# Performance work log

Hardware: AMD Instinct MI355X
Metric: run time of the kernel (lower is better)

## Reference

```python
import jax, jax.numpy as jnp
import numpy as np

B, S, D = 16, 2048, 128

def setup_inputs() -> dict:
    key = jax.random.key(0)
    kq, kk, kv = jax.random.split(key, 3)
    Q = jax.random.normal(kq, (B, S, D), dtype=jnp.float32)
    K = jax.random.normal(kk, (B, S, D), dtype=jnp.float32)
    V = jax.random.normal(kv, (B, S, D), dtype=jnp.float32)
    mask = jnp.ones((B, S), dtype=jnp.int32)  # key padding mask; 0 = masked out
    return {"Q": Q, "K": K, "V": V, "mask": mask}

def reference(Q, K, V, mask):
    scale = jnp.asarray(D ** 0.5, dtype=Q.dtype)
    # scores: [B, Sq, Sk]
    scores = jnp.einsum('bqd,bkd->bqk', Q, K) / scale
    neg_inf = jnp.asarray(float('-inf'), dtype=scores.dtype)
    # mask==0 -> -inf, broadcast over query dim: [B, 1, Sk]
    scores = jnp.where((mask == 0)[:, None, :], neg_inf, scores)
    attn = jax.nn.softmax(scores, axis=-1)
    out = jnp.einsum('bqk,bkd->bqd', attn, V)
    return (out, attn)
```

## Files before the change

kernel.cpp:

```cpp
#include <hip/hip_runtime.h>

#define BB 16
#define SS 2048
#define DD 128
#define SCALE 0.08838834764831845f

typedef __attribute__((ext_vector_type(8))) short bf16x8;
typedef __attribute__((ext_vector_type(4))) float f32x4;

__device__ __forceinline__ unsigned short f2bf(float f) {
    union { float f; unsigned int u; } v; v.f = f;
    unsigned int u = v.u;
    return (unsigned short)((u + 0x7fffu + ((u >> 16) & 1u)) >> 16);
}

__global__ __launch_bounds__(256) void cvt_bf16_kernel(const float* __restrict__ src,
                                                       unsigned short* __restrict__ dst) {
    int idx = (blockIdx.x * 256 + threadIdx.x) * 4;
    float4 f = *(const float4*)(src + idx);
    ushort4 o;
    o.x = f2bf(f.x); o.y = f2bf(f.y); o.z = f2bf(f.z); o.w = f2bf(f.w);
    *(ushort4*)(dst + idx) = o;
}

__global__ __launch_bounds__(256) void transpose_v_kernel(const float* __restrict__ v,
                                                          unsigned short* __restrict__ vt) {
    __shared__ unsigned short sT[64 * 132];
    int b = blockIdx.x >> 5;
    int s0 = (blockIdx.x & 31) * 64;
    int tid = threadIdx.x;
#pragma unroll
    for (int rnd = 0; rnd < 8; ++rnd) {
        int slot = rnd * 256 + tid;
        int row = slot >> 5;
        int c4 = (slot & 31) * 4;
        float4 f = *(const float4*)(v + (size_t)(b * SS + s0 + row) * DD + c4);
        unsigned short* p = &sT[row * 132 + c4];
        p[0] = f2bf(f.x); p[1] = f2bf(f.y); p[2] = f2bf(f.z); p[3] = f2bf(f.w);
    }
    __syncthreads();
#pragma unroll
    for (int rnd = 0; rnd < 4; ++rnd) {
        int slot = rnd * 256 + tid;
        int d = slot >> 3;
        int k8 = (slot & 7) * 8;
        __align__(16) unsigned short tmp[8];
#pragma unroll
        for (int e = 0; e < 8; ++e) tmp[e] = sT[(k8 + e) * 132 + d];
        *(ushort4*)(vt + (size_t)(b * DD + d) * SS + s0 + k8) = *(ushort4*)&tmp[0];
        *(ushort4*)(vt + (size_t)(b * DD + d) * SS + s0 + k8 + 4) = *(ushort4*)&tmp[4];
    }
}

__global__ __launch_bounds__(256) void attn_kernel(const unsigned short* __restrict__ Qb,
                                                   const unsigned short* __restrict__ Kb,
                                                   const unsigned short* __restrict__ Vt,
                                                   const int* __restrict__ mask,
                                                   float* __restrict__ outO,
                                                   float* __restrict__ outA) {
    __shared__ unsigned short sQ[64 * 136];
    __shared__ unsigned short sK[64 * 136];
    __shared__ unsigned short sV[128 * 72];
    __shared__ unsigned short sP[64 * 72];
    __shared__ float sLpart[2][64];
    __shared__ float sLinv[64];
    __shared__ float sMsk[64];

    int bi = blockIdx.x;
    int slot = bi >> 3;
    int b = (bi & 7) * 2 + (slot >> 5);
    int qt = slot & 31;

    int tid = threadIdx.x;
    int wave = tid >> 6, lane = tid & 63, lo = lane & 15, hi = lane >> 4;

    const unsigned short* Qbase = Qb + (size_t)(b * SS + qt * 64) * DD;
#pragma unroll
    for (int rnd = 0; rnd < 4; ++rnd) {
        int sl = rnd * 256 + tid;
        int row = sl >> 4, coff = (sl & 15) * 8;
        *(int4*)&sQ[row * 136 + coff] = *(const int4*)(Qbase + row * DD + coff);
    }
    if (tid < 64) { sLpart[0][tid] = 0.f; sLpart[1][tid] = 0.f; }

    const int r0 = (wave >> 1) * 32;
    const int c0 = (wave & 1) * 32;

    for (int kt = 0; kt < 32; ++kt) {
        __syncthreads();
        const unsigned short* Kbase = Kb + (size_t)(b * SS + kt * 64) * DD;
#pragma unroll
        for (int rnd = 0; rnd < 4; ++rnd) {
            int sl = rnd * 256 + tid;
            int row = sl >> 4, coff = (sl & 15) * 8;
            *(int4*)&sK[row * 136 + coff] = *(const int4*)(Kbase + row * DD + coff);
        }
        if (tid < 64) sMsk[tid] = mask[b * SS + kt * 64 + tid] ? 1.f : 0.f;
        __syncthreads();

        f32x4 acc[2][2];
#pragma unroll
        for (int ii = 0; ii < 2; ++ii)
#pragma unroll
            for (int jj = 0; jj < 2; ++jj) acc[ii][jj] = (f32x4){0.f, 0.f, 0.f, 0.f};
#pragma unroll
        for (int ks = 0; ks < 4; ++ks) {
            bf16x8 af[2], bf[2];
#pragma unroll
            for (int ii = 0; ii < 2; ++ii)
                af[ii] = *(const bf16x8*)&sQ[(r0 + ii * 16 + lo) * 136 + ks * 32 + hi * 8];
#pragma unroll
            for (int jj = 0; jj < 2; ++jj)
                bf[jj] = *(const bf16x8*)&sK[(c0 + jj * 16 + lo) * 136 + ks * 32 + hi * 8];
#pragma unroll
            for (int ii = 0; ii < 2; ++ii)
#pragma unroll
                for (int jj = 0; jj < 2; ++jj)
                    acc[ii][jj] = __builtin_amdgcn_mfma_f32_16x16x32_bf16(af[ii], bf[jj], acc[ii][jj], 0, 0, 0);
        }
        float m0 = sMsk[c0 + lo], m1 = sMsk[c0 + 16 + lo];
#pragma unroll
        for (int ii = 0; ii < 2; ++ii) {
#pragma unroll
            for (int r = 0; r < 4; ++r) {
                float v = __expf(acc[ii][0][r] * SCALE) * m0 + __expf(acc[ii][1][r] * SCALE) * m1;
                v += __shfl_xor(v, 1);
                v += __shfl_xor(v, 2);
                v += __shfl_xor(v, 4);
                v += __shfl_xor(v, 8);
                if (lo == 0) sLpart[wave & 1][r0 + ii * 16 + hi * 4 + r] += v;
            }
        }
    }
    __syncthreads();
    if (tid < 64) sLinv[tid] = 1.f / (sLpart[0][tid] + sLpart[1][tid]);

    f32x4 oacc[4][2];
#pragma unroll
    for (int mi = 0; mi < 4; ++mi)
#pragma unroll
        for (int tj = 0; tj < 2; ++tj) oacc[mi][tj] = (f32x4){0.f, 0.f, 0.f, 0.f};
    const int dv0 = wave * 32;

    for (int kt = 0; kt < 32; ++kt) {
        __syncthreads();
        const unsigned short* Kbase = Kb + (size_t)(b * SS + kt * 64) * DD;
#pragma unroll
        for (int rnd = 0; rnd < 4; ++rnd) {
            int sl = rnd * 256 + tid;
            int row = sl >> 4, coff = (sl & 15) * 8;
            *(int4*)&sK[row * 136 + coff] = *(const int4*)(Kbase + row * DD + coff);
        }
#pragma unroll
        for (int rnd = 0; rnd < 4; ++rnd) {
            int sl = rnd * 256 + tid;
            int row = sl >> 3, koff = (sl & 7) * 8;
            *(int4*)&sV[row * 72 + koff] =
                *(const int4*)(Vt + (size_t)(b * DD + row) * SS + kt * 64 + koff);
        }
        if (tid < 64) sMsk[tid] = mask[b * SS + kt * 64 + tid] ? 1.f : 0.f;
        __syncthreads();

        f32x4 acc[2][2];
#pragma unroll
        for (int ii = 0; ii < 2; ++ii)
#pragma unroll
            for (int jj = 0; jj < 2; ++jj) acc[ii][jj] = (f32x4){0.f, 0.f, 0.f, 0.f};
#pragma unroll
        for (int ks = 0; ks < 4; ++ks) {
            bf16x8 af[2], bf[2];
#pragma unroll
            for (int ii = 0; ii < 2; ++ii)
                af[ii] = *(const bf16x8*)&sQ[(r0 + ii * 16 + lo) * 136 + ks * 32 + hi * 8];
#pragma unroll
            for (int jj = 0; jj < 2; ++jj)
                bf[jj] = *(const bf16x8*)&sK[(c0 + jj * 16 + lo) * 136 + ks * 32 + hi * 8];
#pragma unroll
            for (int ii = 0; ii < 2; ++ii)
#pragma unroll
                for (int jj = 0; jj < 2; ++jj)
                    acc[ii][jj] = __builtin_amdgcn_mfma_f32_16x16x32_bf16(af[ii], bf[jj], acc[ii][jj], 0, 0, 0);
        }
        float m01[2] = {sMsk[c0 + lo], sMsk[c0 + 16 + lo]};
#pragma unroll
        for (int ii = 0; ii < 2; ++ii) {
#pragma unroll
            for (int jj = 0; jj < 2; ++jj) {
#pragma unroll
                for (int r = 0; r < 4; ++r) {
                    int row = r0 + ii * 16 + hi * 4 + r;
                    int col = c0 + jj * 16 + lo;
                    float p = __expf(acc[ii][jj][r] * SCALE) * m01[jj] * sLinv[row];
                    outA[(size_t)(b * SS + qt * 64 + row) * SS + kt * 64 + col] = p;
                    sP[row * 72 + col] = f2bf(p);
                }
            }
        }
        __syncthreads();

#pragma unroll
        for (int ks = 0; ks < 2; ++ks) {
            bf16x8 pa[4], vb[2];
#pragma unroll
            for (int mi = 0; mi < 4; ++mi)
                pa[mi] = *(const bf16x8*)&sP[(mi * 16 + lo) * 72 + ks * 32 + hi * 8];
#pragma unroll
            for (int tj = 0; tj < 2; ++tj)
                vb[tj] = *(const bf16x8*)&sV[(dv0 + tj * 16 + lo) * 72 + ks * 32 + hi * 8];
#pragma unroll
            for (int mi = 0; mi < 4; ++mi)
#pragma unroll
                for (int tj = 0; tj < 2; ++tj)
                    oacc[mi][tj] = __builtin_amdgcn_mfma_f32_16x16x32_bf16(pa[mi], vb[tj], oacc[mi][tj], 0, 0, 0);
        }
    }

#pragma unroll
    for (int mi = 0; mi < 4; ++mi) {
#pragma unroll
        for (int tj = 0; tj < 2; ++tj) {
#pragma unroll
            for (int r = 0; r < 4; ++r) {
                int row = mi * 16 + hi * 4 + r;
                int dv = dv0 + tj * 16 + lo;
                outO[(size_t)(b * SS + qt * 64 + row) * DD + dv] = oacc[mi][tj][r];
            }
        }
    }
}

extern "C" void kernel_launch(void* const* d_in, const int* in_sizes, int n_in,
                              void* d_out, int out_size, void* d_ws, size_t ws_size,
                              hipStream_t stream) {
    const float* Q = (const float*)d_in[0];
    const float* K = (const float*)d_in[1];
    const float* V = (const float*)d_in[2];
    const int* mask = (const int*)d_in[3];

    float* outO = (float*)d_out;
    float* outA = outO + (size_t)BB * SS * DD;

    unsigned short* Qb = (unsigned short*)d_ws;
    unsigned short* Kb = Qb + (size_t)BB * SS * DD;
    unsigned short* Vt = Kb + (size_t)BB * SS * DD;

    int nconv = (BB * SS * DD) / (256 * 4);
    cvt_bf16_kernel<<<nconv, 256, 0, stream>>>(Q, Qb);
    cvt_bf16_kernel<<<nconv, 256, 0, stream>>>(K, Kb);
    transpose_v_kernel<<<BB * (SS / 64), 256, 0, stream>>>(V, Vt);
    attn_kernel<<<BB * (SS / 64), 256, 0, stream>>>(Qb, Kb, Vt, mask, outO, outA);
}
```

Before: 458.5 us.

## Fuse prep kernels, halve query tile, prefetch K/V tiles in registers

Merges the three preprocessing launches into a single prep kernel. The attention kernel's query tile shrinks from 64 to 32 rows, doubling the grid to 1024 blocks, and shared memory is aliased to allow three blocks per CU. The next K and V tiles are loaded into registers while the current tile is computed. Row-sum reductions now stay in registers until the end of the pass, and mask values are read directly from global memory. The main aim is more occupancy and latency hiding on a kernel dominated by writing the attention matrix, at the cost of reading K and V twice as often in total.

```diff
diff --git a/kernel.cpp b/kernel.cpp
--- a/kernel.cpp
+++ b/kernel.cpp
@@ -14,27 +14,34 @@
     return (unsigned short)((u + 0x7fffu + ((u >> 16) & 1u)) >> 16);
 }
 
-__global__ __launch_bounds__(256) void cvt_bf16_kernel(const float* __restrict__ src,
-                                                       unsigned short* __restrict__ dst) {
-    int idx = (blockIdx.x * 256 + threadIdx.x) * 4;
-    float4 f = *(const float4*)(src + idx);
-    ushort4 o;
-    o.x = f2bf(f.x); o.y = f2bf(f.y); o.z = f2bf(f.z); o.w = f2bf(f.w);
-    *(ushort4*)(dst + idx) = o;
-}
-
-__global__ __launch_bounds__(256) void transpose_v_kernel(const float* __restrict__ v,
-                                                          unsigned short* __restrict__ vt) {
+__global__ __launch_bounds__(256) void prep_kernel(const float* __restrict__ Q,
+                                                   const float* __restrict__ K,
+                                                   const float* __restrict__ V,
+                                                   unsigned short* __restrict__ Qb,
+                                                   unsigned short* __restrict__ Kb,
+                                                   unsigned short* __restrict__ Vt) {
+    int bid = blockIdx.x;
+    int tid = threadIdx.x;
+    if (bid < 8192) {
+        const float* src = (bid < 4096) ? Q : K;
+        unsigned short* dst = (bid < 4096) ? Qb : Kb;
+        int idx = ((bid & 4095) * 256 + tid) * 4;
+        float4 f = *(const float4*)(src + idx);
+        ushort4 o;
+        o.x = f2bf(f.x); o.y = f2bf(f.y); o.z = f2bf(f.z); o.w = f2bf(f.w);
+        *(ushort4*)(dst + idx) = o;
+        return;
+    }
     __shared__ unsigned short sT[64 * 132];
-    int b = blockIdx.x >> 5;
-    int s0 = (blockIdx.x & 31) * 64;
-    int tid = threadIdx.x;
+    int tb = bid - 8192;
+    int b = tb >> 5;
+    int s0 = (tb & 31) * 64;
 #pragma unroll
     for (int rnd = 0; rnd < 8; ++rnd) {
         int slot = rnd * 256 + tid;
         int row = slot >> 5;
         int c4 = (slot & 31) * 4;
-        float4 f = *(const float4*)(v + (size_t)(b * SS + s0 + row) * DD + c4);
+        float4 f = *(const float4*)(V + (size_t)(b * SS + s0 + row) * DD + c4);
         unsigned short* p = &sT[row * 132 + c4];
         p[0] = f2bf(f.x); p[1] = f2bf(f.y); p[2] = f2bf(f.z); p[3] = f2bf(f.w);
     }
@@ -47,183 +54,213 @@
         __align__(16) unsigned short tmp[8];
 #pragma unroll
         for (int e = 0; e < 8; ++e) tmp[e] = sT[(k8 + e) * 132 + d];
-        *(ushort4*)(vt + (size_t)(b * DD + d) * SS + s0 + k8) = *(ushort4*)&tmp[0];
-        *(ushort4*)(vt + (size_t)(b * DD + d) * SS + s0 + k8 + 4) = *(ushort4*)&tmp[4];
-    }
-}
-
-__global__ __launch_bounds__(256) void attn_kernel(const unsigned short* __restrict__ Qb,
-                                                   const unsigned short* __restrict__ Kb,
-                                                   const unsigned short* __restrict__ Vt,
-                                                   const int* __restrict__ mask,
-                                                   float* __restrict__ outO,
-                                                   float* __restrict__ outA) {
-    __shared__ unsigned short sQ[64 * 136];
-    __shared__ unsigned short sK[64 * 136];
-    __shared__ unsigned short sV[128 * 72];
-    __shared__ unsigned short sP[64 * 72];
-    __shared__ float sLpart[2][64];
-    __shared__ float sLinv[64];
-    __shared__ float sMsk[64];
+        *(ushort4*)(Vt + (size_t)(b * DD + d) * SS + s0 + k8) = *(ushort4*)&tmp[0];
+        *(ushort4*)(Vt + (size_t)(b * DD + d) * SS + s0 + k8 + 4) = *(ushort4*)&tmp[4];
+    }
+}
+
+__global__ __launch_bounds__(256, 3) void attn_kernel(const unsigned short* __restrict__ Qb,
+                                                      const unsigned short* __restrict__ Kb,
+                                                      const unsigned short* __restrict__ Vt,
+                                                      const int* __restrict__ mask,
+                                                      float* __restrict__ outO,
+                                                      float* __restrict__ outA) {
+    __shared__ __align__(16) char smem[44544];
+    unsigned short* sQ = (unsigned short*)smem;
+    unsigned short* sK = (unsigned short*)(smem + 8704);
+    unsigned short* sP = sK;
+    unsigned short* sV = (unsigned short*)(smem + 8704 + 17408);
+    float* sLpart = (float*)sV;
 
     int bi = blockIdx.x;
     int slot = bi >> 3;
-    int b = (bi & 7) * 2 + (slot >> 5);
-    int qt = slot & 31;
+    int b = (bi & 7) * 2 + (slot >> 6);
+    int qt = slot & 63;
 
     int tid = threadIdx.x;
     int wave = tid >> 6, lane = tid & 63, lo = lane & 15, hi = lane >> 4;
-
-    const unsigned short* Qbase = Qb + (size_t)(b * SS + qt * 64) * DD;
-#pragma unroll
-    for (int rnd = 0; rnd < 4; ++rnd) {
+    const int r0 = (wave >> 1) * 16;
+    const int c0 = (wave & 1) * 32;
+
+    const unsigned short* KbB = Kb + (size_t)b * SS * DD;
+    const unsigned short* VtB = Vt + (size_t)b * DD * SS;
+    const int* maskB = mask + b * SS;
+
+    const unsigned short* Qbase = Qb + (size_t)(b * SS + qt * 32) * DD;
+#pragma unroll
+    for (int rnd = 0; rnd < 2; ++rnd) {
         int sl = rnd * 256 + tid;
         int row = sl >> 4, coff = (sl & 15) * 8;
         *(int4*)&sQ[row * 136 + coff] = *(const int4*)(Qbase + row * DD + coff);
     }
-    if (tid < 64) { sLpart[0][tid] = 0.f; sLpart[1][tid] = 0.f; }
-
-    const int r0 = (wave >> 1) * 32;
-    const int c0 = (wave & 1) * 32;
-
+
+    int4 kreg[4];
+#pragma unroll
+    for (int rnd = 0; rnd < 4; ++rnd) {
+        int sl = rnd * 256 + tid;
+        int row = sl >> 4, coff = (sl & 15) * 8;
+        kreg[rnd] = *(const int4*)(KbB + row * DD + coff);
+    }
+    float regsum[4] = {0.f, 0.f, 0.f, 0.f};
     for (int kt = 0; kt < 32; ++kt) {
         __syncthreads();
-        const unsigned short* Kbase = Kb + (size_t)(b * SS + kt * 64) * DD;
 #pragma unroll
         for (int rnd = 0; rnd < 4; ++rnd) {
             int sl = rnd * 256 + tid;
             int row = sl >> 4, coff = (sl & 15) * 8;
-            *(int4*)&sK[row * 136 + coff] = *(const int4*)(Kbase + row * DD + coff);
-        }
-        if (tid < 64) sMsk[tid] = mask[b * SS + kt * 64 + tid] ? 1.f : 0.f;
-        __syncthreads();
-
-        f32x4 acc[2][2];
-#pragma unroll
-        for (int ii = 0; ii < 2; ++ii)
-#pragma unroll
-            for (int jj = 0; jj < 2; ++jj) acc[ii][jj] = (f32x4){0.f, 0.f, 0.f, 0.f};
+            *(int4*)&sK[row * 136 + coff] = kreg[rnd];
+        }
+        float m0 = maskB[kt * 64 + c0 + lo] ? 1.f : 0.f;
+        float m1 = maskB[kt * 64 + c0 + 16 + lo] ? 1.f : 0.f;
+        if (kt < 31) {
+#pragma unroll
+            for (int rnd = 0; rnd < 4; ++rnd) {
+                int sl = rnd * 256 + tid;
+                int row = sl >> 4, coff = (sl & 15) * 8;
+                kreg[rnd] = *(const int4*)(KbB + ((kt + 1) * 64 + row) * DD + coff);
+            }
+        }
+        __syncthreads();
+        f32x4 acc[2];
+        acc[0] = (f32x4){0.f, 0.f, 0.f, 0.f};
+        acc[1] = (f32x4){0.f, 0.f, 0.f, 0.f};
 #pragma unroll
         for (int ks = 0; ks < 4; ++ks) {
-            bf16x8 af[2], bf[2];
-#pragma unroll
-            for (int ii = 0; ii < 2; ++ii)
-                af[ii] = *(const bf16x8*)&sQ[(r0 + ii * 16 + lo) * 136 + ks * 32 + hi * 8];
-#pragma unroll
-            for (int jj = 0; jj < 2; ++jj)
-                bf[jj] = *(const bf16x8*)&sK[(c0 + jj * 16 + lo) * 136 + ks * 32 + hi * 8];
-#pragma unroll
-            for (int ii = 0; ii < 2; ++ii)
-#pragma unroll
-                for (int jj = 0; jj < 2; ++jj)
-                    acc[ii][jj] = __builtin_amdgcn_mfma_f32_16x16x32_bf16(af[ii], bf[jj], acc[ii][jj], 0, 0, 0);
-        }
-        float m0 = sMsk[c0 + lo], m1 = sMsk[c0 + 16 + lo];
-#pragma unroll
-        for (int ii = 0; ii < 2; ++ii) {
-#pragma unroll
-            for (int r = 0; r < 4; ++r) {
-                float v = __expf(acc[ii][0][r] * SCALE) * m0 + __expf(acc[ii][1][r] * SCALE) * m1;
-                v += __shfl_xor(v, 1);
-                v += __shfl_xor(v, 2);
-                v += __shfl_xor(v, 4);
-                v += __shfl_xor(v, 8);
-                if (lo == 0) sLpart[wave & 1][r0 + ii * 16 + hi * 4 + r] += v;
-            }
-        }
+            bf16x8 af = *(const bf16x8*)&sQ[(r0 + lo) * 136 + ks * 32 + hi * 8];
+            bf16x8 bf0 = *(const bf16x8*)&sK[(c0 + lo) * 136 + ks * 32 + hi * 8];
+            bf16x8 bf1 = *(const bf16x8*)&sK[(c0 + 16 + lo) * 136 + ks * 32 + hi * 8];
+            acc[0] = __builtin_amdgcn_mfma_f32_16x16x32_bf16(af, bf0, acc[0], 0, 0, 0);
+            acc[1] = __builtin_amdgcn_mfma_f32_16x16x32_bf16(af, bf1, acc[1], 0, 0, 0);
+        }
+#pragma unroll
+        for (int r = 0; r < 4; ++r)
+            regsum[r] += __expf(acc[0][r] * SCALE) * m0 + __expf(acc[1][r] * SCALE) * m1;
+    }
+#pragma unroll
+    for (int r = 0; r < 4; ++r) {
+        float v = regsum[r];
+        v += __shfl_xor(v, 1);
+        v += __shfl_xor(v, 2);
+        v += __shfl_xor(v, 4);
+        v += __shfl_xor(v, 8);
+        regsum[r] = v;
+    }
+    if (lo == 0) {
+#pragma unroll
+        for (int r = 0; r < 4; ++r) sLpart[(wave & 1) * 32 + r0 + hi * 4 + r] = regsum[r];
     }
     __syncthreads();
-    if (tid < 64) sLinv[tid] = 1.f / (sLpart[0][tid] + sLpart[1][tid]);
-
-    f32x4 oacc[4][2];
-#pragma unroll
-    for (int mi = 0; mi < 4; ++mi)
+    float linv[4];
+#pragma unroll
+    for (int r = 0; r < 4; ++r) {
+        int row = r0 + hi * 4 + r;
+        linv[r] = 1.f / (sLpart[row] + sLpart[32 + row]);
+    }
+
+    int4 kreg2[4], vreg[4];
+#pragma unroll
+    for (int rnd = 0; rnd < 4; ++rnd) {
+        int sl = rnd * 256 + tid;
+        int row = sl >> 4, coff = (sl & 15) * 8;
+        kreg2[rnd] = *(const int4*)(KbB + row * DD + coff);
+    }
+#pragma unroll
+    for (int rnd = 0; rnd < 4; ++rnd) {
+        int sl = rnd * 256 + tid;
+        int row = sl >> 3, koff = (sl & 7) * 8;
+        vreg[rnd] = *(const int4*)(VtB + (size_t)row * SS + koff);
+    }
+    f32x4 oacc[2][2];
+#pragma unroll
+    for (int mi = 0; mi < 2; ++mi)
 #pragma unroll
         for (int tj = 0; tj < 2; ++tj) oacc[mi][tj] = (f32x4){0.f, 0.f, 0.f, 0.f};
     const int dv0 = wave * 32;
+    float* outArow = outA + (size_t)(b * SS + qt * 32) * SS;
 
     for (int kt = 0; kt < 32; ++kt) {
         __syncthreads();
-        const unsigned short* Kbase = Kb + (size_t)(b * SS + kt * 64) * DD;
 #pragma unroll
         for (int rnd = 0; rnd < 4; ++rnd) {
             int sl = rnd * 256 + tid;
             int row = sl >> 4, coff = (sl & 15) * 8;
-            *(int4*)&sK[row * 136 + coff] = *(const int4*)(Kbase + row * DD + coff);
+            *(int4*)&sK[row * 136 + coff] = kreg2[rnd];
         }
 #pragma unroll
         for (int rnd = 0; rnd < 4; ++rnd) {
             int sl = rnd * 256 + tid;
             int row = sl >> 3, koff = (sl & 7) * 8;
-            *(int4*)&sV[row * 72 + koff] =
-                *(const int4*)(Vt + (size_t)(b * DD + row) * SS + kt * 64 + koff);
-        }
-        if (tid < 64) sMsk[tid] = mask[b * SS + kt * 64 + tid] ? 1.f : 0.f;
-        __syncthreads();
-
-        f32x4 acc[2][2];
-#pragma unroll
-        for (int ii = 0; ii < 2; ++ii)
-#pragma unroll
-            for (int jj = 0; jj < 2; ++jj) acc[ii][jj] = (f32x4){0.f, 0.f, 0.f, 0.f};
+            *(int4*)&sV[row * 72 + koff] = vreg[rnd];
+        }
+        float m0 = maskB[kt * 64 + c0 + lo] ? 1.f : 0.f;
+        float m1 = maskB[kt * 64 + c0 + 16 + lo] ? 1.f : 0.f;
+        if (kt < 31) {
+#pragma unroll
+            for (int rnd = 0; rnd < 4; ++rnd) {
+                int sl = rnd * 256 + tid;
+                int row = sl >> 4, coff = (sl & 15) * 8;
+                kreg2[rnd] = *(const int4*)(KbB + ((kt + 1) * 64 + row) * DD + coff);
+            }
+#pragma unroll
+            for (int rnd = 0; rnd < 4; ++rnd) {
+                int sl = rnd * 256 + tid;
+                int row = sl >> 3, koff = (sl & 7) * 8;
+                vreg[rnd] = *(const int4*)(VtB + (size_t)row * SS + (kt + 1) * 64 + koff);
+            }
+        }
+        __syncthreads();
+        f32x4 acc[2];
+        acc[0] = (f32x4){0.f, 0.f, 0.f, 0.f};
+        acc[1] = (f32x4){0.f, 0.f, 0.f, 0.f};
 #pragma unroll
         for (int ks = 0; ks < 4; ++ks) {
-            bf16x8 af[2], bf[2];
-#pragma unroll
-            for (int ii = 0; ii < 2; ++ii)
-                af[ii] = *(const bf16x8*)&sQ[(r0 + ii * 16 + lo) * 136 + ks * 32 + hi * 8];
-#pragma unroll
-            for (int jj = 0; jj < 2; ++jj)
-                bf[jj] = *(const bf16x8*)&sK[(c0 + jj * 16 + lo) * 136 + ks * 32 + hi * 8];
-#pragma unroll
-            for (int ii = 0; ii < 2; ++ii)
-#pragma unroll
-                for (int jj = 0; jj < 2; ++jj)
-                    acc[ii][jj] = __builtin_amdgcn_mfma_f32_16x16x32_bf16(af[ii], bf[jj], acc[ii][jj], 0, 0, 0);
-        }
-        float m01[2] = {sMsk[c0 + lo], sMsk[c0 + 16 + lo]};
-#pragma unroll
-        for (int ii = 0; ii < 2; ++ii) {
-#pragma unroll
-            for (int jj = 0; jj < 2; ++jj) {
-#pragma unroll
-                for (int r = 0; r < 4; ++r) {
-                    int row = r0 + ii * 16 + hi * 4 + r;
-                    int col = c0 + jj * 16 + lo;
-                    float p = __expf(acc[ii][jj][r] * SCALE) * m01[jj] * sLinv[row];
-                    outA[(size_t)(b * SS + qt * 64 + row) * SS + kt * 64 + col] = p;
-                    sP[row * 72 + col] = f2bf(p);
-                }
-            }
-        }
-        __syncthreads();
-
+            bf16x8 af = *(const bf16x8*)&sQ[(r0 + lo) * 136 + ks * 32 + hi * 8];
+            bf16x8 bf0 = *(const bf16x8*)&sK[(c0 + lo) * 136 + ks * 32 + hi * 8];
+            bf16x8 bf1 = *(const bf16x8*)&sK[(c0 + 16 + lo) * 136 + ks * 32 + hi * 8];
+            acc[0] = __builtin_amdgcn_mfma_f32_16x16x32_bf16(af, bf0, acc[0], 0, 0, 0);
+            acc[1] = __builtin_amdgcn_mfma_f32_16x16x32_bf16(af, bf1, acc[1], 0, 0, 0);
+        }
+        __syncthreads();
+#pragma unroll
+        for (int jj = 0; jj < 2; ++jj) {
+            float mj = jj ? m1 : m0;
+#pragma unroll
+            for (int r = 0; r < 4; ++r) {
+                int row = r0 + hi * 4 + r;
+                int col = c0 + jj * 16 + lo;
+                float p = __expf(acc[jj][r] * SCALE) * mj * linv[r];
+                outArow[(size_t)row * SS + kt * 64 + col] = p;
+                sP[row * 72 + col] = f2bf(p);
+            }
+        }
+        __syncthreads();
 #pragma unroll
         for (int ks = 0; ks < 2; ++ks) {
-            bf16x8 pa[4], vb[2];
-#pragma unroll
-            for (int mi = 0; mi < 4; ++mi)
+            bf16x8 pa[2], vb[2];
+#pragma unroll
+            for (int mi = 0; mi < 2; ++mi)
                 pa[mi] = *(const bf16x8*)&sP[(mi * 16 + lo) * 72 + ks * 32 + hi * 8];
 #pragma unroll
             for (int tj = 0; tj < 2; ++tj)
                 vb[tj] = *(const bf16x8*)&sV[(dv0 + tj * 16 + lo) * 72 + ks * 32 + hi * 8];
 #pragma unroll
-            for (int mi = 0; mi < 4; ++mi)
+            for (int mi = 0; mi < 2; ++mi)
 #pragma unroll
                 for (int tj = 0; tj < 2; ++tj)
                     oacc[mi][tj] = __builtin_amdgcn_mfma_f32_16x16x32_bf16(pa[mi], vb[tj], oacc[mi][tj], 0, 0, 0);
         }
     }
 
-#pragma unroll
-    for (int mi = 0; mi < 4; ++mi) {
+    float* outOrow = outO + (size_t)(b * SS + qt * 32) * DD;
+#pragma unroll
+    for (int mi = 0; mi < 2; ++mi) {
 #pragma unroll
         for (int tj = 0; tj < 2; ++tj) {
 #pragma unroll
             for (int r = 0; r < 4; ++r) {
                 int row = mi * 16 + hi * 4 + r;
                 int dv = dv0 + tj * 16 + lo;
-                outO[(size_t)(b * SS + qt * 64 + row) * DD + dv] = oacc[mi][tj][r];
+                outOrow[(size_t)row * DD + dv] = oacc[mi][tj][r];
             }
         }
     }
@@ -244,9 +281,6 @@
     unsigned short* Kb = Qb + (size_t)BB * SS * DD;
     unsigned short* Vt = Kb + (size_t)BB * SS * DD;
 
-    int nconv = (BB * SS * DD) / (256 * 4);
-    cvt_bf16_kernel<<<nconv, 256, 0, stream>>>(Q, Qb);
-    cvt_bf16_kernel<<<nconv, 256, 0, stream>>>(K, Kb);
-    transpose_v_kernel<<<BB * (SS / 64), 256, 0, stream>>>(V, Vt);
-    attn_kernel<<<BB * (SS / 64), 256, 0, stream>>>(Qb, Kb, Vt, mask, outO, outA);
-}
+    prep_kernel<<<8192 + BB * (SS / 64), 256, 0, stream>>>(Q, K, V, Qb, Kb, Vt);
+    attn_kernel<<<BB * (SS / 32), 256, 0, stream>>>(Qb, Kb, Vt, mask, outO, outA);
+}
```

New measurement: 719.9 us. 57.0% more time.
